# Kernel tuning notes

Hardware: AMD Instinct MI355X
Metric: run time of the kernel (lower is better)

The kernel has to match this reference:

```python
import jax, jax.numpy as jnp
import numpy as np

SIGMA_XY = 15.0
SIGMA_RGB = 0.125
B, C, H, W = 1, 1, 96, 96


def setup_inputs() -> dict:
    key = jax.random.key(0)
    k1, k2 = jax.random.split(key)
    inp = jax.random.uniform(k1, (B, C, H, W), dtype=jnp.float32)   # segmentation probs in [0,1]
    img = jax.random.uniform(k2, (B, 3, H, W), dtype=jnp.float32)   # RGB in [0,1]
    return {"input": inp, "image": img}


def _crf_loss_single(s, img, pos):
    # s: [C, N] probs, img: [3, N] colors, pos: [N, 2] scaled xy coords
    feat = jnp.concatenate([pos, img.T / SIGMA_RGB], axis=1)        # [N, 5] joint bilateral features
    sq = jnp.sum(feat * feat, axis=1)                                # [N]
    d2 = sq[:, None] + sq[None, :] - 2.0 * (feat @ feat.T)           # [N, N] squared feature distance
    Wm = jnp.exp(-0.5 * jnp.maximum(d2, 0.0))                        # [N, N] Gaussian bilateral affinity
    # dense CRF relaxed Potts loss: sum_c s_c^T W (1 - s_c)
    return jnp.sum((Wm @ (1.0 - s.T)) * s.T)


def reference(input, image):
    b, c, h, w = input.shape
    n = h * w
    yy, xx = jnp.meshgrid(jnp.arange(h, dtype=input.dtype),
                          jnp.arange(w, dtype=input.dtype), indexing="ij")
    pos = jnp.stack([xx, yy], axis=-1).reshape(n, 2) / SIGMA_XY      # [N, 2]
    s = input.reshape(b, c, n)
    img = image.reshape(b, 3, n)
    losses = jax.vmap(lambda sv, iv: _crf_loss_single(sv, iv, pos))(s, img)
    return jnp.sum(losses) / n                                        # per-pixel normalized scalar loss
```

## Files before the change

kernel.cpp:

```cpp
#include <hip/hip_runtime.h>

#define NPTS  9216
#define WIDTH 96
#define IPT   4
#define IBLK  (256*IPT)
#define NIB   9
#define JTILE 128
#define NJB   72

#define KSCALE 1.2011224087864498f

typedef _Float16 half2v __attribute__((ext_vector_type(2)));
union H2F { half2v h; float f; };

__global__ __launch_bounds__(256)
void crf_feat_kernel(const float* __restrict__ s,
                     const float* __restrict__ img,
                     float4* __restrict__ arrJ,
                     float4* __restrict__ arrI,
                     float* __restrict__ out) {
    int p = blockIdx.x * 256 + threadIdx.x;
    if (p == 0) out[0] = 0.0f;
    if (p >= NPTS) return;
    int y = p / WIDTH;
    int x = p - y * WIDTH;
    float sv = s[p];
    float xs = (float)x * (KSCALE / 15.0f);
    float ys = (float)y * (KSCALE / 15.0f);
    float rs = img[p]          * (8.0f * KSCALE);
    float gs = img[NPTS + p]   * (8.0f * KSCALE);
    float bs = img[2*NPTS + p] * (8.0f * KSCALE);
    _Float16 xh = (_Float16)xs, yh = (_Float16)ys;
    _Float16 rh = (_Float16)rs, gh = (_Float16)gs, bh = (_Float16)bs;
    float xr = (float)xh, yr = (float)yh, rr = (float)rh, gr = (float)gh, br = (float)bh;
    float hs = -0.5f * (xr*xr + yr*yr + rr*rr + gr*gr + br*br);
    float hsl = hs + __builtin_amdgcn_logf(1.0f - sv);

    H2F xy; xy.h = half2v{xh, yh};
    H2F rg; rg.h = half2v{rh, gh};
    H2F b0; b0.h = half2v{bh, (_Float16)0.0f};

    float4 rj, ri;
    rj.x = xy.f; rj.y = rg.f; rj.z = b0.f; rj.w = hsl;
    ri.x = xy.f; ri.y = rg.f; ri.z = b0.f; ri.w = hs;
    arrJ[p] = rj;
    arrI[p] = ri;
}

__global__ __launch_bounds__(256)
void crf_pair_kernel(const float4* __restrict__ arrJ,
                     const float4* __restrict__ arrI,
                     const float* __restrict__ s,
                     float* __restrict__ out) {
    __shared__ float4 shJ[JTILE];
    __shared__ float wavesum[4];

    const int tid   = threadIdx.x;
    const int ibase = blockIdx.x * IBLK;
    const int jbase = blockIdx.y * JTILE;

    if (tid < JTILE) shJ[tid] = arrJ[jbase + tid];

    half2v xyi[IPT], rgi[IPT], b0i[IPT];
    float  hsi[IPT], svi[IPT];
    #pragma unroll
    for (int k = 0; k < IPT; ++k) {
        int i = ibase + k * 256 + tid;
        float4 r = arrI[i];
        H2F a; a.f = r.x; xyi[k] = a.h;
        H2F b; b.f = r.y; rgi[k] = b.h;
        H2F c; c.f = r.z; b0i[k] = c.h;
        hsi[k] = r.w;
        svi[k] = s[i];
    }

    __syncthreads();

    float acc[IPT];
    #pragma unroll
    for (int k = 0; k < IPT; ++k) acc[k] = 0.0f;

    #pragma unroll 4
    for (int j = 0; j < JTILE; ++j) {
        float4 rj = shJ[j];
        H2F a; a.f = rj.x;
        H2F b; b.f = rj.y;
        H2F c; c.f = rj.z;
        const half2v xyj = a.h, rgj = b.h, b0j = c.h;
        const float hslj = rj.w;
        #pragma unroll
        for (int k = 0; k < IPT; ++k) {
            float e = hsi[k] + hslj;
            e = __builtin_amdgcn_fdot2(xyi[k], xyj, e, false);
            e = __builtin_amdgcn_fdot2(rgi[k], rgj, e, false);
            e = __builtin_amdgcn_fdot2(b0i[k], b0j, e, false);
            acc[k] += __builtin_amdgcn_exp2f(e);
        }
    }

    float t = acc[0]*svi[0] + acc[1]*svi[1] + acc[2]*svi[2] + acc[3]*svi[3];

    #pragma unroll
    for (int off = 32; off > 0; off >>= 1)
        t += __shfl_down(t, off, 64);
    if ((tid & 63) == 0) wavesum[tid >> 6] = t;
    __syncthreads();
    if (tid == 0) {
        float r = wavesum[0] + wavesum[1] + wavesum[2] + wavesum[3];
        atomicAdd(out, r * (1.0f / (float)NPTS));
    }
}

extern "C" void kernel_launch(void* const* d_in, const int* in_sizes, int n_in,
                              void* d_out, int out_size, void* d_ws, size_t ws_size,
                              hipStream_t stream) {
    const float* s   = (const float*)d_in[0];
    const float* img = (const float*)d_in[1];
    float* out = (float*)d_out;

    float4* arrJ = (float4*)d_ws;
    float4* arrI = arrJ + NPTS;

    crf_feat_kernel<<<NPTS/256, 256, 0, stream>>>(s, img, arrJ, arrI, out);
    dim3 grid(NIB, NJB);
    crf_pair_kernel<<<grid, 256, 0, stream>>>(arrJ, arrI, s, out);
}
```

Baseline: 78.13 us.

## Exploit affinity symmetry to compute only upper-triangle tile pairs

Rewrites the pairwise loss using the symmetry of the Gaussian affinity matrix. Each unordered pair contributes w*(s_i + s_j - 2 s_i s_j), so only tiles with jb >= ib are evaluated and diagonal tiles are halved. This roughly halves the exp evaluations, at the cost of an extra FMA per pair. Half of the launched blocks exit immediately. The j data is now read straight from global memory (served by cache) instead of being staged in LDS, and blocks shrink to 128 threads with 2 i-points each.

Result: slower. 91.59 us (+17.2%).

```diff
diff --git a/kernel.cpp b/kernel.cpp
--- a/kernel.cpp
+++ b/kernel.cpp
@@ -2,11 +2,9 @@
 
 #define NPTS  9216
 #define WIDTH 96
-#define IPT   4
-#define IBLK  (256*IPT)
-#define NIB   9
-#define JTILE 128
-#define NJB   72
+#define TILE  256
+#define NT    36
+#define IPT   2
 
 #define KSCALE 1.2011224087864498f
 
@@ -16,8 +14,8 @@
 __global__ __launch_bounds__(256)
 void crf_feat_kernel(const float* __restrict__ s,
                      const float* __restrict__ img,
-                     float4* __restrict__ arrJ,
-                     float4* __restrict__ arrI,
+                     float4* __restrict__ arrF,
+                     float* __restrict__ arrS,
                      float* __restrict__ out) {
     int p = blockIdx.x * 256 + threadIdx.x;
     if (p == 0) out[0] = 0.0f;
@@ -34,81 +32,76 @@
     _Float16 rh = (_Float16)rs, gh = (_Float16)gs, bh = (_Float16)bs;
     float xr = (float)xh, yr = (float)yh, rr = (float)rh, gr = (float)gh, br = (float)bh;
     float hs = -0.5f * (xr*xr + yr*yr + rr*rr + gr*gr + br*br);
-    float hsl = hs + __builtin_amdgcn_logf(1.0f - sv);
 
     H2F xy; xy.h = half2v{xh, yh};
     H2F rg; rg.h = half2v{rh, gh};
     H2F b0; b0.h = half2v{bh, (_Float16)0.0f};
 
-    float4 rj, ri;
-    rj.x = xy.f; rj.y = rg.f; rj.z = b0.f; rj.w = hsl;
-    ri.x = xy.f; ri.y = rg.f; ri.z = b0.f; ri.w = hs;
-    arrJ[p] = rj;
-    arrI[p] = ri;
+    float4 r;
+    r.x = xy.f; r.y = rg.f; r.z = b0.f; r.w = hs;
+    arrF[p] = r;
+    arrS[p] = sv;
 }
 
-__global__ __launch_bounds__(256)
-void crf_pair_kernel(const float4* __restrict__ arrJ,
-                     const float4* __restrict__ arrI,
-                     const float* __restrict__ s,
+__global__ __launch_bounds__(128)
+void crf_pair_kernel(const float4* __restrict__ arrF,
+                     const float* __restrict__ arrS,
                      float* __restrict__ out) {
-    __shared__ float4 shJ[JTILE];
-    __shared__ float wavesum[4];
+    const int ib = blockIdx.x;
+    const int jb = blockIdx.y;
+    if (jb < ib) return;
 
+    __shared__ float wavesum[2];
     const int tid   = threadIdx.x;
-    const int ibase = blockIdx.x * IBLK;
-    const int jbase = blockIdx.y * JTILE;
-
-    if (tid < JTILE) shJ[tid] = arrJ[jbase + tid];
+    const int ibase = ib * TILE;
+    const int jbase = jb * TILE;
 
     half2v xyi[IPT], rgi[IPT], b0i[IPT];
     float  hsi[IPT], svi[IPT];
     #pragma unroll
     for (int k = 0; k < IPT; ++k) {
-        int i = ibase + k * 256 + tid;
-        float4 r = arrI[i];
+        int i = ibase + k * 128 + tid;
+        float4 r = arrF[i];
         H2F a; a.f = r.x; xyi[k] = a.h;
         H2F b; b.f = r.y; rgi[k] = b.h;
         H2F c; c.f = r.z; b0i[k] = c.h;
         hsi[k] = r.w;
-        svi[k] = s[i];
+        svi[k] = arrS[i];
     }
 
-    __syncthreads();
-
-    float acc[IPT];
-    #pragma unroll
-    for (int k = 0; k < IPT; ++k) acc[k] = 0.0f;
+    float acc[IPT] = {0.0f, 0.0f};
 
     #pragma unroll 4
-    for (int j = 0; j < JTILE; ++j) {
-        float4 rj = shJ[j];
-        H2F a; a.f = rj.x;
-        H2F b; b.f = rj.y;
-        H2F c; c.f = rj.z;
+    for (int j = 0; j < TILE; ++j) {
+        const float4 fj = arrF[jbase + j];
+        const float  sj = arrS[jbase + j];
+        const float  cj = 1.0f - 2.0f * sj;
+        H2F a; a.f = fj.x;
+        H2F b; b.f = fj.y;
+        H2F c; c.f = fj.z;
         const half2v xyj = a.h, rgj = b.h, b0j = c.h;
-        const float hslj = rj.w;
         #pragma unroll
         for (int k = 0; k < IPT; ++k) {
-            float e = hsi[k] + hslj;
+            float e = hsi[k] + fj.w;
             e = __builtin_amdgcn_fdot2(xyi[k], xyj, e, false);
             e = __builtin_amdgcn_fdot2(rgi[k], rgj, e, false);
             e = __builtin_amdgcn_fdot2(b0i[k], b0j, e, false);
-            acc[k] += __builtin_amdgcn_exp2f(e);
+            float w = __builtin_amdgcn_exp2f(e);
+            float g = fmaf(svi[k], cj, sj);
+            acc[k] = fmaf(w, g, acc[k]);
         }
     }
 
-    float t = acc[0]*svi[0] + acc[1]*svi[1] + acc[2]*svi[2] + acc[3]*svi[3];
+    float t = acc[0] + acc[1];
+    const float factor = (ib == jb) ? 0.5f : 1.0f;
+    t *= factor * (1.0f / (float)NPTS);
 
     #pragma unroll
     for (int off = 32; off > 0; off >>= 1)
         t += __shfl_down(t, off, 64);
     if ((tid & 63) == 0) wavesum[tid >> 6] = t;
     __syncthreads();
-    if (tid == 0) {
-        float r = wavesum[0] + wavesum[1] + wavesum[2] + wavesum[3];
-        atomicAdd(out, r * (1.0f / (float)NPTS));
-    }
+    if (tid == 0) atomicAdd(out, wavesum[0] + wavesum[1]);
 }
 
 extern "C" void kernel_launch(void* const* d_in, const int* in_sizes, int n_in,
@@ -118,10 +111,10 @@
     const float* img = (const float*)d_in[1];
     float* out = (float*)d_out;
 
-    float4* arrJ = (float4*)d_ws;
-    float4* arrI = arrJ + NPTS;
+    float4* arrF = (float4*)d_ws;
+    float*  arrS = (float*)(arrF + NPTS);
 
-    crf_feat_kernel<<<NPTS/256, 256, 0, stream>>>(s, img, arrJ, arrI, out);
-    dim3 grid(NIB, NJB);
-    crf_pair_kernel<<<grid, 256, 0, stream>>>(arrJ, arrI, s, out);
+    crf_feat_kernel<<<NPTS/256, 256, 0, stream>>>(s, img, arrF, arrS, out);
+    dim3 grid(NT, NT);
+    crf_pair_kernel<<<grid, 128, 0, stream>>>(arrF, arrS, out);
 }
```
